# Optimization experiments

Measured on AMD Instinct MI355X. Metric: run time of the kernel, lower is better.

## Reference

```python
import jax, jax.numpy as jnp
import numpy as np

MAT_MODE = [[0, 1], [0, 2], [1, 2]]
VEC_MODE = [2, 1, 0]


def _bilinear(plane, gx, gy):
    """grid_sample(align_corners=True, bilinear) on a single plane.
    plane: [C, H, W]; gx, gy: [N] normalized coords in [-1, 1] (x indexes W, y indexes H).
    Returns [C, N]."""
    C, H, W = plane.shape
    x = (gx + 1.0) * 0.5 * (W - 1)
    y = (gy + 1.0) * 0.5 * (H - 1)
    x0 = jnp.clip(jnp.floor(x), 0, W - 2).astype(jnp.int32)
    y0 = jnp.clip(jnp.floor(y), 0, H - 2).astype(jnp.int32)
    wx = x - x0
    wy = y - y0
    v00 = plane[:, y0, x0]
    v01 = plane[:, y0, x0 + 1]
    v10 = plane[:, y0 + 1, x0]
    v11 = plane[:, y0 + 1, x0 + 1]
    return (v00 * (1 - wx) * (1 - wy) + v01 * wx * (1 - wy)
            + v10 * (1 - wx) * wy + v11 * wx * wy)


def setup_inputs() -> dict:
    key = jax.random.key(0)
    k1, k2, k3 = jax.random.split(key, 3)
    N = 2097152
    C = 8          # density_n_comp
    RES = 300      # num_levels
    APP = 32       # app_dim
    inputs = jax.random.uniform(k1, (N, 3), dtype=jnp.float32)  # in [0,1) subset of [-1,1]
    planes = 0.1 * jax.random.normal(k2, (3, C, RES, RES), dtype=jnp.float32)
    W = jax.random.normal(k3, (APP, 3 * C), dtype=jnp.float32) * (1.0 / np.sqrt(3 * C))
    return {"inputs": inputs, "planes": planes, "W": W, "size": 1}


def reference(inputs, planes, W, size):
    x = inputs / size
    # coordinates are detached in the original (grid_sample grid is .detach()ed)
    c = jax.lax.stop_gradient(x)
    feats = []
    for i in range(3):  # 3 structurally distinct planes (fixed small loop)
        m0, m1 = MAT_MODE[i]
        v = VEC_MODE[i]
        # plane sample: grid (x=c[m0], y=c[m1]) over plane [C, res(m1), res(m0)]
        p = _bilinear(planes[i], c[:, m0], c[:, m1])
        # NOTE: source code (faithfully reproduced) samples the *plane* again
        # with grid (x=0, y=c[vec]) for the "line" features.
        l = _bilinear(planes[i], jnp.zeros_like(c[:, v]), c[:, v])
        feats.append(p * l)  # [C, N]
    feat = jnp.concatenate(feats, axis=0)  # [3C, N]
    return feat.T @ W.T  # [N, app_dim], Linear with no bias
```

## Files before the change

### kernel.cpp

```cpp
#include <hip/hip_runtime.h>

#define RES 300
#define NC 8
#define KF 24
#define AP 32
#define PX 152
#define PBASE 148
#define LTROWS 152
#define LTS 12
#define CH 4

typedef float f4 __attribute__((ext_vector_type(4)));
typedef _Float16 h8 __attribute__((ext_vector_type(8)));

__global__ __launch_bounds__(256) void build_packed2(const float* __restrict__ planes,
                                                     _Float16* __restrict__ packed2) {
    int idx = blockIdx.x * blockDim.x + threadIdx.x;
    if (idx >= 3 * PX * PX) return;
    int px = idx % PX;
    int t  = idx / PX;
    int py = t % PX;
    int i  = t / PX;
    int x  = PBASE + px;
    int y0 = PBASE + py;
    int y1 = min(y0 + 1, RES - 1);
    h8 v0, v1;
#pragma unroll
    for (int c = 0; c < NC; ++c) {
        v0[c] = (_Float16)planes[((i * NC + c) * RES + y0) * RES + x];
        v1[c] = (_Float16)planes[((i * NC + c) * RES + y1) * RES + x];
    }
    _Float16* dst = packed2 + (size_t)idx * 16;
    *(h8*)(dst + 0) = v0;
    *(h8*)(dst + 8) = v1;
}

__global__ __launch_bounds__(256) void build_lt(const float* __restrict__ planes,
                                                float* __restrict__ lt) {
    int idx = blockIdx.x * blockDim.x + threadIdx.x;
    if (idx >= 3 * LTROWS * NC) return;
    int c = idx % NC;
    int t = idx / NC;
    int r = t % LTROWS;
    int i = t / LTROWS;
    int y = PBASE + r;
    const float* row = planes + ((i * NC + c) * RES + y) * RES;
    lt[idx] = 0.5f * (row[149] + row[150]);
}

__device__ __forceinline__ float decode_scalar(const void* p) {
    int b = *(const int*)p;
    if (b > 0 && b < (1 << 23)) return (float)b;
    return __int_as_float(b);
}

__global__ __launch_bounds__(256, 4) void tensorf_main(
    const float* __restrict__ inputs, const float* __restrict__ W,
    const _Float16* __restrict__ packed2, const float* __restrict__ lt,
    const void* __restrict__ size_p, float* __restrict__ out, int N)
{
    __shared__ __align__(16) float lt_s[3 * LTROWS * LTS];
    __shared__ __align__(16) float ob[64 * 36];

    int t = threadIdx.x;
    for (int idx = t; idx < 3 * LTROWS * NC; idx += 256) {
        int c  = idx & 7;
        int rr = idx >> 3;
        lt_s[rr * LTS + c] = lt[idx];
    }
    __syncthreads();

    float inv_s = 1.0f / decode_scalar(size_p);

    for (int chunk = 0; chunk < CH; ++chunk) {
        int n0 = (blockIdx.x * CH + chunk) * 256;
        int n  = n0 + t;

        float r_out[AP];
        if (n < N) {
            float c0 = inputs[3 * n + 0] * inv_s;
            float c1 = inputs[3 * n + 1] * inv_s;
            float c2 = inputs[3 * n + 2] * inv_s;

            float gxA[3] = {c0, c0, c1};
            float gyA[3] = {c1, c2, c2};
            float gvA[3] = {c2, c1, c0};

            h8    tx[3][4];
            float wxA[3], wyA[3], wvA[3];
            int   pyvA[3];
#pragma unroll
            for (int i = 0; i < 3; ++i) {
                float xx = (gxA[i] + 1.0f) * (0.5f * (RES - 1));
                float yy = (gyA[i] + 1.0f) * (0.5f * (RES - 1));
                float xf = fminf(fmaxf(floorf(xx), 0.0f), (float)(RES - 2));
                float yf = fminf(fmaxf(floorf(yy), 0.0f), (float)(RES - 2));
                int   x0 = (int)xf, y0 = (int)yf;
                wxA[i] = xx - xf;
                wyA[i] = yy - yf;
                int px = min(max(x0 - PBASE, 0), PX - 2);
                int py = min(max(y0 - PBASE, 0), PX - 2);

                const _Float16* ep = packed2 + ((size_t)((i * PX + py) * PX + px)) * 16;
                tx[i][0] = *(const h8*)(ep + 0);
                tx[i][1] = *(const h8*)(ep + 8);
                tx[i][2] = *(const h8*)(ep + 16);
                tx[i][3] = *(const h8*)(ep + 24);

                float yv  = (gvA[i] + 1.0f) * (0.5f * (RES - 1));
                float yvf = fminf(fmaxf(floorf(yv), 0.0f), (float)(RES - 2));
                wvA[i]  = yv - yvf;
                pyvA[i] = min(max((int)yvf - PBASE, 0), LTROWS - 2);
            }

            float feat[KF];
#pragma unroll
            for (int i = 0; i < 3; ++i) {
                const float* l0 = lt_s + (i * LTROWS + pyvA[i]) * LTS;
                f4 e0 = *(const f4*)(l0 + 0);
                f4 e1 = *(const f4*)(l0 + 4);
                f4 g0 = *(const f4*)(l0 + LTS + 0);
                f4 g1 = *(const f4*)(l0 + LTS + 4);
                float lv0[NC] = {e0.x, e0.y, e0.z, e0.w, e1.x, e1.y, e1.z, e1.w};
                float lv1[NC] = {g0.x, g0.y, g0.z, g0.w, g1.x, g1.y, g1.z, g1.w};

                float wx = wxA[i], wy = wyA[i], wv = wvA[i];
                float w11 = wx * wy;
                float w01 = wx - w11;
                float w10 = wy - w11;
                float w00 = 1.0f - wx - w10;
#pragma unroll
                for (int c = 0; c < NC; ++c) {
                    float p = w00 * (float)tx[i][0][c];
                    p = fmaf(w10, (float)tx[i][1][c], p);
                    p = fmaf(w01, (float)tx[i][2][c], p);
                    p = fmaf(w11, (float)tx[i][3][c], p);
                    float l = fmaf(wv, lv1[c] - lv0[c], lv0[c]);
                    feat[i * NC + c] = p * l;
                }
            }

#pragma unroll
            for (int a = 0; a < AP; ++a) {
                float s = 0.0f;
#pragma unroll
                for (int k = 0; k < KF; ++k)
                    s = fmaf(feat[k], W[a * KF + k], s);
                r_out[a] = s;
            }
        }

#pragma unroll
        for (int h = 0; h < 4; ++h) {
            if ((t >> 6) == h && n < N) {
                int tr = t & 63;
#pragma unroll
                for (int a4 = 0; a4 < 8; ++a4)
                    *(f4*)&ob[tr * 36 + a4 * 4] =
                        f4{r_out[a4 * 4 + 0], r_out[a4 * 4 + 1],
                           r_out[a4 * 4 + 2], r_out[a4 * 4 + 3]};
            }
            __syncthreads();
            int base_n = n0 + h * 64;
#pragma unroll
            for (int k = 0; k < 2; ++k) {
                int j   = k * 256 + t;
                int row = j >> 3;
                int c4  = j & 7;
                int gn  = base_n + row;
                if (gn < N) {
                    f4 v = *(const f4*)&ob[row * 36 + c4 * 4];
                    __builtin_nontemporal_store(
                        v, (f4*)(out + (size_t)gn * AP + c4 * 4));
                }
            }
            __syncthreads();
        }
    }
}

extern "C" void kernel_launch(void* const* d_in, const int* in_sizes, int n_in,
                              void* d_out, int out_size, void* d_ws, size_t ws_size,
                              hipStream_t stream) {
    const float* inputs = (const float*)d_in[0];
    const float* planes = (const float*)d_in[1];
    const float* W      = (const float*)d_in[2];
    const void*  size_p = d_in[3];
    float* out = (float*)d_out;
    int N = in_sizes[0] / 3;

    _Float16* packed2 = (_Float16*)d_ws;
    float*    ltbuf   = (float*)(packed2 + 3 * PX * PX * 16);

    int ppos = 3 * PX * PX;
    build_packed2<<<(ppos + 255) / 256, 256, 0, stream>>>(planes, packed2);
    int lpos = 3 * LTROWS * NC;
    build_lt<<<(lpos + 255) / 256, 256, 0, stream>>>(planes, ltbuf);
    int nblocks = (N + 256 * CH - 1) / (256 * CH);
    tensorf_main<<<nblocks, 256, 0, stream>>>(inputs, W, packed2, ltbuf,
                                              size_p, out, N);
}
```

Before: 112.1 us.

## Cooperatively gather bilinear texels across lane quads with shuffles

Each group of four lanes now fetches the four 16-byte corner texels of each neighbour's sample, so one quad issues contiguous 64-byte loads per point instead of each lane doing four scattered loads. Weighted partial sums are then reduced across the quad with xor shuffles, and each lane keeps its own result. Out-of-range lanes are clamped to the last point so every lane takes part in the shuffles. This aims at better load coalescing and fewer memory transactions, at the cost of many extra cross-lane shuffle instructions and redundant multiplies.

```diff
diff --git a/kernel.cpp b/kernel.cpp
--- a/kernel.cpp
+++ b/kernel.cpp
@@ -71,83 +71,101 @@
     __syncthreads();
 
     float inv_s = 1.0f / decode_scalar(size_p);
+    int lane  = t & 63;
+    int m     = lane & 3;
+    int qbase = lane & ~3;
+
+    const char* pbase = (const char*)packed2;
 
     for (int chunk = 0; chunk < CH; ++chunk) {
         int n0 = (blockIdx.x * CH + chunk) * 256;
         int n  = n0 + t;
+        int np = min(n, N - 1);
+
+        float c0 = inputs[3 * np + 0] * inv_s;
+        float c1 = inputs[3 * np + 1] * inv_s;
+        float c2 = inputs[3 * np + 2] * inv_s;
+
+        float gxA[3] = {c0, c0, c1};
+        float gyA[3] = {c1, c2, c2};
+        float gvA[3] = {c2, c1, c0};
+
+        int   offA[3];
+        float wxA[3], wyA[3], wvA[3];
+        int   pyvA[3];
+#pragma unroll
+        for (int i = 0; i < 3; ++i) {
+            float xx = (gxA[i] + 1.0f) * (0.5f * (RES - 1));
+            float yy = (gyA[i] + 1.0f) * (0.5f * (RES - 1));
+            float xf = fminf(fmaxf(floorf(xx), 0.0f), (float)(RES - 2));
+            float yf = fminf(fmaxf(floorf(yy), 0.0f), (float)(RES - 2));
+            int   x0 = (int)xf, y0 = (int)yf;
+            wxA[i] = xx - xf;
+            wyA[i] = yy - yf;
+            int px = min(max(x0 - PBASE, 0), PX - 2);
+            int py = min(max(y0 - PBASE, 0), PX - 2);
+            offA[i] = ((i * PX + py) * PX + px) * 32;
+
+            float yv  = (gvA[i] + 1.0f) * (0.5f * (RES - 1));
+            float yvf = fminf(fmaxf(floorf(yv), 0.0f), (float)(RES - 2));
+            wvA[i]  = yv - yvf;
+            pyvA[i] = min(max((int)yvf - PBASE, 0), LTROWS - 2);
+        }
+
+        h8 tex[3][4];
+#pragma unroll
+        for (int i = 0; i < 3; ++i)
+#pragma unroll
+            for (int r = 0; r < 4; ++r) {
+                int off_s = __shfl(offA[i], qbase + r, 64);
+                tex[i][r] = *(const h8*)(pbase + off_s + m * 16);
+            }
+
+        float pown[3][NC];
+#pragma unroll
+        for (int i = 0; i < 3; ++i)
+#pragma unroll
+            for (int r = 0; r < 4; ++r) {
+                float wx_s = __shfl(wxA[i], qbase + r, 64);
+                float wy_s = __shfl(wyA[i], qbase + r, 64);
+                float wmx = (m & 2) ? wx_s : (1.0f - wx_s);
+                float wmy = (m & 1) ? wy_s : (1.0f - wy_s);
+                float wm  = wmx * wmy;
+#pragma unroll
+                for (int c = 0; c < NC; ++c) {
+                    float p = wm * (float)tex[i][r][c];
+                    p += __shfl_xor(p, 1, 64);
+                    p += __shfl_xor(p, 2, 64);
+                    if (m == r) pown[i][c] = p;
+                }
+            }
+
+        float feat[KF];
+#pragma unroll
+        for (int i = 0; i < 3; ++i) {
+            const float* l0 = lt_s + (i * LTROWS + pyvA[i]) * LTS;
+            f4 e0 = *(const f4*)(l0 + 0);
+            f4 e1 = *(const f4*)(l0 + 4);
+            f4 g0 = *(const f4*)(l0 + LTS + 0);
+            f4 g1 = *(const f4*)(l0 + LTS + 4);
+            float lv0[NC] = {e0.x, e0.y, e0.z, e0.w, e1.x, e1.y, e1.z, e1.w};
+            float lv1[NC] = {g0.x, g0.y, g0.z, g0.w, g1.x, g1.y, g1.z, g1.w};
+            float wv = wvA[i];
+#pragma unroll
+            for (int c = 0; c < NC; ++c) {
+                float l = fmaf(wv, lv1[c] - lv0[c], lv0[c]);
+                feat[i * NC + c] = pown[i][c] * l;
+            }
+        }
 
         float r_out[AP];
-        if (n < N) {
-            float c0 = inputs[3 * n + 0] * inv_s;
-            float c1 = inputs[3 * n + 1] * inv_s;
-            float c2 = inputs[3 * n + 2] * inv_s;
-
-            float gxA[3] = {c0, c0, c1};
-            float gyA[3] = {c1, c2, c2};
-            float gvA[3] = {c2, c1, c0};
-
-            h8    tx[3][4];
-            float wxA[3], wyA[3], wvA[3];
-            int   pyvA[3];
-#pragma unroll
-            for (int i = 0; i < 3; ++i) {
-                float xx = (gxA[i] + 1.0f) * (0.5f * (RES - 1));
-                float yy = (gyA[i] + 1.0f) * (0.5f * (RES - 1));
-                float xf = fminf(fmaxf(floorf(xx), 0.0f), (float)(RES - 2));
-                float yf = fminf(fmaxf(floorf(yy), 0.0f), (float)(RES - 2));
-                int   x0 = (int)xf, y0 = (int)yf;
-                wxA[i] = xx - xf;
-                wyA[i] = yy - yf;
-                int px = min(max(x0 - PBASE, 0), PX - 2);
-                int py = min(max(y0 - PBASE, 0), PX - 2);
-
-                const _Float16* ep = packed2 + ((size_t)((i * PX + py) * PX + px)) * 16;
-                tx[i][0] = *(const h8*)(ep + 0);
-                tx[i][1] = *(const h8*)(ep + 8);
-                tx[i][2] = *(const h8*)(ep + 16);
-                tx[i][3] = *(const h8*)(ep + 24);
-
-                float yv  = (gvA[i] + 1.0f) * (0.5f * (RES - 1));
-                float yvf = fminf(fmaxf(floorf(yv), 0.0f), (float)(RES - 2));
-                wvA[i]  = yv - yvf;
-                pyvA[i] = min(max((int)yvf - PBASE, 0), LTROWS - 2);
-            }
-
-            float feat[KF];
-#pragma unroll
-            for (int i = 0; i < 3; ++i) {
-                const float* l0 = lt_s + (i * LTROWS + pyvA[i]) * LTS;
-                f4 e0 = *(const f4*)(l0 + 0);
-                f4 e1 = *(const f4*)(l0 + 4);
-                f4 g0 = *(const f4*)(l0 + LTS + 0);
-                f4 g1 = *(const f4*)(l0 + LTS + 4);
-                float lv0[NC] = {e0.x, e0.y, e0.z, e0.w, e1.x, e1.y, e1.z, e1.w};
-                float lv1[NC] = {g0.x, g0.y, g0.z, g0.w, g1.x, g1.y, g1.z, g1.w};
-
-                float wx = wxA[i], wy = wyA[i], wv = wvA[i];
-                float w11 = wx * wy;
-                float w01 = wx - w11;
-                float w10 = wy - w11;
-                float w00 = 1.0f - wx - w10;
-#pragma unroll
-                for (int c = 0; c < NC; ++c) {
-                    float p = w00 * (float)tx[i][0][c];
-                    p = fmaf(w10, (float)tx[i][1][c], p);
-                    p = fmaf(w01, (float)tx[i][2][c], p);
-                    p = fmaf(w11, (float)tx[i][3][c], p);
-                    float l = fmaf(wv, lv1[c] - lv0[c], lv0[c]);
-                    feat[i * NC + c] = p * l;
-                }
-            }
-
-#pragma unroll
-            for (int a = 0; a < AP; ++a) {
-                float s = 0.0f;
-#pragma unroll
-                for (int k = 0; k < KF; ++k)
-                    s = fmaf(feat[k], W[a * KF + k], s);
-                r_out[a] = s;
-            }
+#pragma unroll
+        for (int a = 0; a < AP; ++a) {
+            float s = 0.0f;
+#pragma unroll
+            for (int k = 0; k < KF; ++k)
+                s = fmaf(feat[k], W[a * KF + k], s);
+            r_out[a] = s;
         }
 
 #pragma unroll
```

Result: slower. 191.4 us (+70.7%).
